# Kernel tuning notes

Hardware: AMD Instinct MI355X
Metric: run time of the kernel (lower is better)

Reference implementation:

```python
import jax, jax.numpy as jnp
import numpy as np

DIM = 64
N_VAR = 60000
N_CON = 40000
N = 100000
E = 500000
NL = 4  # number of MIPGNN layers


def setup_inputs() -> dict:
    key = jax.random.key(0)
    ks = iter(jax.random.split(key, 64))
    def nrm(shape, scale=0.1):
        return jax.random.normal(next(ks), shape, jnp.float32) * scale
    inp = {}
    inp["var_node_features"] = nrm((N_VAR, 1), 1.0)
    inp["con_node_features"] = nrm((N_CON, 1), 1.0)
    inp["edge_features"] = nrm((N, 1), 1.0)
    inp["edge_index"] = jax.random.randint(next(ks), (2, E), 0, N)
    inp["edge_types"] = jax.random.randint(next(ks), (E,), 0, 2)
    inp["assoc_var"] = jnp.arange(N_VAR)
    inp["assoc_con"] = jnp.arange(N_VAR, N)
    # var/con input MLPs
    inp["var_mlp_w1"] = nrm((1, DIM - 2)); inp["var_mlp_b1"] = jnp.zeros((DIM - 2,), jnp.float32)
    inp["var_mlp_w2"] = nrm((DIM - 2, DIM - 2)); inp["var_mlp_b2"] = jnp.zeros((DIM - 2,), jnp.float32)
    inp["con_mlp_w1"] = nrm((1, DIM - 1)); inp["con_mlp_b1"] = jnp.zeros((DIM - 1,), jnp.float32)
    inp["con_mlp_w2"] = nrm((DIM - 1, DIM - 1)); inp["con_mlp_b2"] = jnp.zeros((DIM - 1,), jnp.float32)
    # per-layer MIPGNN params (stacked over NL layers)
    inp["htv_w1"] = nrm((NL, DIM, DIM)); inp["htv_b1"] = jnp.zeros((NL, DIM), jnp.float32)
    inp["htv_w2"] = nrm((NL, DIM, 1)); inp["htv_b2"] = jnp.zeros((NL, 1), jnp.float32)
    inp["w_cons"] = nrm((NL, DIM - 2, DIM - 2))
    inp["w_vars"] = nrm((NL, DIM, DIM))
    inp["bias"] = nrm((NL, DIM))
    # final dense head
    inp["fc1_w"] = nrm((5 * DIM, DIM)); inp["fc1_b"] = jnp.zeros((DIM,), jnp.float32)
    inp["fc2_w"] = nrm((DIM, DIM)); inp["fc2_b"] = jnp.zeros((DIM,), jnp.float32)
    inp["fc3_w"] = nrm((DIM, DIM)); inp["fc3_b"] = jnp.zeros((DIM,), jnp.float32)
    inp["fc4_w"] = nrm((DIM, 1)); inp["fc4_b"] = jnp.zeros((1,), jnp.float32)
    return inp


def _mlp2_relu(x, w1, b1, w2, b2):
    return jax.nn.relu(x @ w1 + b1) @ w2 + b2


def _net_forward(var_node_features, con_node_features, edge_features,
                 var_mlp_w1, var_mlp_b1, var_mlp_w2, var_mlp_b2,
                 con_mlp_w1, con_mlp_b1, con_mlp_w2, con_mlp_b2,
                 htv_w1, htv_b1, htv_w2, htv_b2, w_cons, w_vars, bias,
                 fc1_w, fc1_b, fc2_w, fc2_b, fc3_w, fc3_b, fc4_w, fc4_b,
                 edge_index, edge_types, assoc_var, assoc_con):
    # build initial node features: [var_mlp(v), v, 1] and [con_mlp(c), c]
    ones = jnp.ones_like(var_node_features)
    n = jnp.concatenate([_mlp2_relu(var_node_features, var_mlp_w1, var_mlp_b1, var_mlp_w2, var_mlp_b2),
                         var_node_features, ones], axis=-1)  # [N_VAR, DIM]
    e = jnp.concatenate([_mlp2_relu(con_node_features, con_mlp_w1, con_mlp_b1, con_mlp_w2, con_mlp_b2),
                         con_node_features], axis=-1)         # [N_CON, DIM]
    x = jnp.zeros((N, DIM), jnp.float32).at[assoc_var].set(n).at[assoc_con].set(e)

    src, dst = edge_index[0], edge_index[1]
    et0 = (edge_types == 0)[:, None]          # [E, 1]
    ef_src = edge_features[src]               # [E, 1] (edge_feature indexed by source node)

    xs = [x]
    for l in range(NL):
        xj = xs[-1][src]                      # gather [E, DIM]
        h = jax.nn.sigmoid(xj @ htv_w1[l] + htv_b1[l])
        var_assign = (h @ htv_w2[l] + htv_b2[l]) * ef_src   # [E, 1]
        out0 = jnp.concatenate([xj[:, :-2] @ w_cons[l], xj[:, -2:-1], var_assign], axis=-1)
        out1 = xj @ w_vars[l]
        msg = jnp.where(et0, out0, out1)      # edge-type branching
        aggr = jax.ops.segment_sum(msg, dst, num_segments=N) + bias[l]
        xs.append(jax.nn.relu(aggr))

    xcat = jnp.concatenate(xs, axis=-1)[assoc_var]   # [N_VAR, 5*DIM]
    h = jax.nn.relu(xcat @ fc1_w + fc1_b)
    h = jax.nn.relu(h @ fc2_w + fc2_b)
    h = jax.nn.relu(h @ fc3_w + fc3_b)
    return (h @ fc4_w + fc4_b).squeeze(-1)           # [N_VAR]


def reference(var_node_features, con_node_features, edge_features,
              edge_index, edge_types, assoc_var, assoc_con,
              var_mlp_w1, var_mlp_b1, var_mlp_w2, var_mlp_b2,
              con_mlp_w1, con_mlp_b1, con_mlp_w2, con_mlp_b2,
              htv_w1, htv_b1, htv_w2, htv_b2, w_cons, w_vars, bias,
              fc1_w, fc1_b, fc2_w, fc2_b, fc3_w, fc3_b, fc4_w, fc4_b):
    return _net_forward(var_node_features, con_node_features, edge_features,
                        var_mlp_w1, var_mlp_b1, var_mlp_w2, var_mlp_b2,
                        con_mlp_w1, con_mlp_b1, con_mlp_w2, con_mlp_b2,
                        htv_w1, htv_b1, htv_w2, htv_b2, w_cons, w_vars, bias,
                        fc1_w, fc1_b, fc2_w, fc2_b, fc3_w, fc3_b, fc4_w, fc4_b,
                        edge_index, edge_types, assoc_var, assoc_con)
```

## Files before the change

### kernel.cpp

```cpp
#include <hip/hip_runtime.h>
#include <hip/hip_bf16.h>

typedef unsigned int u32;
typedef unsigned short u16;
typedef __attribute__((ext_vector_type(8))) short frag8;
typedef __attribute__((ext_vector_type(4))) float f32x4;

#define NNODE 100000
#define NVAR  60000
#define NCON  40000
#define NEDGE 500000
#define SLOTCAP 32
#define VAR_BLOCKS 469
#define CON_BLOCKS 313

#define WP_NODE(l)  ((l) * 24576)
#define WP_VARW2    98304
#define WP_CONW2    106496
#define WP_FC1(ph)  (114688 + (ph) * 20480)
#define WP_FC2      155648
#define WP_FC3      163840
#define PREP_TOTAL  86016

__device__ __forceinline__ u16 f2bf(float f) {
  u32 u = __float_as_uint(f);
  u32 r = (u + 0x7fffu + ((u >> 16) & 1u)) >> 16;
  return (u16)r;
}
__device__ __forceinline__ float bf2f(u16 u) { return __uint_as_float(((u32)u) << 16); }
__device__ __forceinline__ float cvlo(u32 p) { return __uint_as_float(p << 16); }
__device__ __forceinline__ float cvhi(u32 p) { return __uint_as_float(p & 0xffff0000u); }
__device__ __forceinline__ float sigmoidf_(float x) {
  return __builtin_amdgcn_rcpf(1.0f + __expf(-x));
}

__global__ __launch_bounds__(256) void k_prep(
    const float* __restrict__ hw1, const float* __restrict__ wco,
    const float* __restrict__ wva, const float* __restrict__ vw2,
    const float* __restrict__ cw2, const float* __restrict__ f1w,
    const float* __restrict__ f2w, const float* __restrict__ f3w,
    u16* __restrict__ wp)
{
  int g = blockIdx.x * 256 + threadIdx.x;
  if (g >= PREP_TOTAL) return;
  float w; u16* base; int k, n, fr_hi, fr_lo;
  if (g < 49152) {
    int l = g / 12288, e = g % 12288;
    base = wp + WP_NODE(l);
    if (e < 4096) {
      k = e >> 6; n = e & 63;
      w = hw1[l * 4096 + e];
      int ksp = k >> 5, nt = n >> 4;
      fr_hi = ksp * 4 + nt;
      fr_lo = (2 + ksp) * 4 + nt;
    } else {
      int e2 = e - 4096;
      int kk = e2 >> 6; n = e2 & 63;
      if (kk < 64) w = (kk < 62 && n < 62) ? wco[l * 3844 + kk * 62 + n] : 0.f;
      else         w = wva[l * 4096 + (kk - 64) * 64 + n];
      k = kk;
      int kkp = kk >> 5, nt = n >> 4;
      fr_hi = 16 + kkp * 4 + nt;
      fr_lo = 16 + (4 + kkp) * 4 + nt;
    }
  } else if (g < 53248) {
    int idx = g - 49152; k = idx >> 6; n = idx & 63;
    w = (k < 62 && n < 62) ? vw2[k * 62 + n] : 0.f;
    base = wp + WP_VARW2;
    int ksp = k >> 5, nt = n >> 4;
    fr_hi = ksp * 4 + nt; fr_lo = (2 + ksp) * 4 + nt;
  } else if (g < 57344) {
    int idx = g - 53248; k = idx >> 6; n = idx & 63;
    w = (k < 63 && n < 63) ? cw2[k * 63 + n] : 0.f;
    base = wp + WP_CONW2;
    int ksp = k >> 5, nt = n >> 4;
    fr_hi = ksp * 4 + nt; fr_lo = (2 + ksp) * 4 + nt;
  } else if (g < 77824) {
    int e = g - 57344; int kk = e >> 6; n = e & 63;
    int ph = (kk >= 160); k = kk - ph * 160;
    w = f1w[(size_t)kk * 64 + n];
    base = wp + WP_FC1(ph);
    int ksp = k >> 5, nt = n >> 4;
    fr_hi = ksp * 4 + nt; fr_lo = (5 + ksp) * 4 + nt;
  } else if (g < 81920) {
    int idx = g - 77824; k = idx >> 6; n = idx & 63;
    w = f2w[idx];
    base = wp + WP_FC2;
    int ksp = k >> 5, nt = n >> 4;
    fr_hi = ksp * 4 + nt; fr_lo = (2 + ksp) * 4 + nt;
  } else {
    int idx = g - 81920; k = idx >> 6; n = idx & 63;
    w = f3w[idx];
    base = wp + WP_FC3;
    int ksp = k >> 5, nt = n >> 4;
    fr_hi = ksp * 4 + nt; fr_lo = (2 + ksp) * 4 + nt;
  }
  u16 hi = f2bf(w);
  u16 lo = f2bf(w - bf2f(hi));
  int lane = (n & 15) | (((k & 31) >> 3) << 4);
  int j = k & 7;
  base[fr_hi * 512 + lane * 8 + j] = hi;
  base[fr_lo * 512 + lane * 8 + j] = lo;
}

__global__ __launch_bounds__(256) void k_init(
    const float* __restrict__ vf, const float* __restrict__ cf,
    const int* __restrict__ avar, const int* __restrict__ acon,
    const float* __restrict__ vw1, const float* __restrict__ vb1, const float* __restrict__ vb2,
    const float* __restrict__ cw1, const float* __restrict__ cb1, const float* __restrict__ cb2,
    const u16* __restrict__ wp, u16* __restrict__ x0, int* __restrict__ cnt)
{
  for (int i = blockIdx.x * 256 + threadIdx.x; i < NNODE; i += gridDim.x * 256) cnt[i] = 0;

  const bool isVar = blockIdx.x < VAR_BLOCKS;
  const int bbase = isVar ? blockIdx.x : (blockIdx.x - VAR_BLOCKS);
  const int nItems = isVar ? NVAR : NCON;
  const int KD = isVar ? 62 : 63;
  const float* in  = isVar ? vf : cf;
  const int*   asc = isVar ? avar : acon;
  const float* w1  = isVar ? vw1 : cw1;
  const float* b1  = isVar ? vb1 : cb1;
  const float* b2  = isVar ? vb2 : cb2;
  const u16*   src = wp + (isVar ? WP_VARW2 : WP_CONW2);

  __shared__ u16 sB[16 * 512];
  __shared__ float sw1[64], sb1[64], sb2[64];
  {
    const uint4* s4 = reinterpret_cast<const uint4*>(src);
    uint4* d4 = reinterpret_cast<uint4*>(sB);
    for (int i = threadIdx.x; i < 1024; i += 256) d4[i] = s4[i];
  }
  if (threadIdx.x < 64) {
    int t = threadIdx.x;
    sw1[t] = (t < KD) ? w1[t] : 0.f;
    sb1[t] = (t < KD) ? b1[t] : 0.f;
    sb2[t] = (t < KD) ? b2[t] : 0.f;
  }
  __syncthreads();

  int wid = threadIdx.x >> 6, lane = threadIdx.x & 63;
  long ib = ((long)bbase * 4 + wid) * 32;
  if (ib >= nItems) return;
  int l15 = lane & 15, lg = lane >> 4;

  float w1r[16], b1r[16];
#pragma unroll
  for (int ks = 0; ks < 2; ++ks)
#pragma unroll
    for (int j = 0; j < 8; ++j) {
      int k = 32 * ks + 8 * lg + j;
      w1r[ks * 8 + j] = sw1[k]; b1r[ks * 8 + j] = sb1[k];
    }

  float v0 = in[ib + l15], v1 = in[ib + 16 + l15];
  frag8 hh[2][2], hl[2][2];
#pragma unroll
  for (int np = 0; np < 2; ++np) {
    float v = np ? v1 : v0;
#pragma unroll
    for (int ks = 0; ks < 2; ++ks) {
      frag8 th, tl;
#pragma unroll
      for (int j = 0; j < 8; ++j) {
        float h = fmaxf(fmaf(v, w1r[ks * 8 + j], b1r[ks * 8 + j]), 0.f);
        u16 hi = f2bf(h);
        u16 lo = f2bf(h - bf2f(hi));
        th[j] = (short)hi; tl[j] = (short)lo;
      }
      hh[np][ks] = th; hl[np][ks] = tl;
    }
  }

  const f32x4 z = {0.f, 0.f, 0.f, 0.f};
  f32x4 acc[4][2];
#pragma unroll
  for (int m = 0; m < 4; ++m)
#pragma unroll
    for (int np = 0; np < 2; ++np) acc[m][np] = z;

#pragma unroll
  for (int ks = 0; ks < 2; ++ks)
#pragma unroll
    for (int m = 0; m < 4; ++m) {
      frag8 bh = *reinterpret_cast<const frag8*>(&sB[((ks * 4 + m) * 512) + lane * 8]);
      frag8 bl = *reinterpret_cast<const frag8*>(&sB[(((2 + ks) * 4 + m) * 512) + lane * 8]);
#pragma unroll
      for (int np = 0; np < 2; ++np) {
        acc[m][np] = __builtin_amdgcn_mfma_f32_16x16x32_bf16(bh, hh[np][ks], acc[m][np], 0, 0, 0);
        acc[m][np] = __builtin_amdgcn_mfma_f32_16x16x32_bf16(bh, hl[np][ks], acc[m][np], 0, 0, 0);
        acc[m][np] = __builtin_amdgcn_mfma_f32_16x16x32_bf16(bl, hh[np][ks], acc[m][np], 0, 0, 0);
      }
    }

#pragma unroll
  for (int np = 0; np < 2; ++np) {
    long r = asc[ib + 16 * np + l15];
    float vv = np ? v1 : v0;
    u16* orow = x0 + r * 64;
#pragma unroll
    for (int m = 0; m < 4; ++m) {
      float o[4];
#pragma unroll
      for (int rr = 0; rr < 4; ++rr) o[rr] = acc[m][np][rr] + sb2[16 * m + 4 * lg + rr];
      if (m == 3 && lg == 3) {
        if (isVar) { o[2] = vv; o[3] = 1.0f; } else { o[3] = vv; }
      }
      u32 p0 = (u32)f2bf(o[0]) | ((u32)f2bf(o[1]) << 16);
      u32 p1 = (u32)f2bf(o[2]) | ((u32)f2bf(o[3]) << 16);
      *reinterpret_cast<uint2*>(orow + 16 * m + 4 * lg) = make_uint2(p0, p1);
    }
  }
}

__global__ __launch_bounds__(256) void k_scatter(
    const int* __restrict__ src, const int* __restrict__ dst,
    const int* __restrict__ et, int* __restrict__ cnt, int* __restrict__ slots)
{
  int e = blockIdx.x * 256 + threadIdx.x;
  if (e >= NEDGE) return;
  int d = dst[e];
  int pos = atomicAdd(&cnt[d], 1);
  if (pos < SLOTCAP) slots[d * SLOTCAP + pos] = src[e] | ((et[e] & 1) << 20);
}

__global__ __launch_bounds__(256) void k_gate(
    const u16* __restrict__ x, const float* __restrict__ ef,
    const u16* __restrict__ wsrc,
    const float* __restrict__ b1, const float* __restrict__ w2,
    const float* __restrict__ b2, float* __restrict__ va)
{
  __shared__ u16 sB[16 * 512];
  __shared__ float sb1[64], sw2[64];
  {
    const uint4* s4 = reinterpret_cast<const uint4*>(wsrc);
    uint4* d4 = reinterpret_cast<uint4*>(sB);
    for (int i = threadIdx.x; i < 1024; i += 256) d4[i] = s4[i];
  }
  if (threadIdx.x < 64) { sb1[threadIdx.x] = b1[threadIdx.x]; sw2[threadIdx.x] = w2[threadIdx.x]; }
  __syncthreads();

  int wid = threadIdx.x >> 6, lane = threadIdx.x & 63;
  long nb = ((long)blockIdx.x * 4 + wid) * 32;
  if (nb >= NNODE) return;
  int l15 = lane & 15, lg = lane >> 4;

  frag8 xf[2][2];
#pragma unroll
  for (int np = 0; np < 2; ++np) {
    const u16* base = x + (nb + 16 * np + l15) * 64 + 8 * lg;
    xf[np][0] = *reinterpret_cast<const frag8*>(base);
    xf[np][1] = *reinterpret_cast<const frag8*>(base + 32);
  }

  const f32x4 z = {0.f, 0.f, 0.f, 0.f};
  f32x4 acc[4][2];
#pragma unroll
  for (int m = 0; m < 4; ++m)
#pragma unroll
    for (int np = 0; np < 2; ++np) acc[m][np] = z;

#pragma unroll
  for (int ks = 0; ks < 2; ++ks)
#pragma unroll
    for (int m = 0; m < 4; ++m) {
      frag8 bh = *reinterpret_cast<const frag8*>(&sB[((ks * 4 + m) * 512) + lane * 8]);
      frag8 bl = *reinterpret_cast<const frag8*>(&sB[(((2 + ks) * 4 + m) * 512) + lane * 8]);
#pragma unroll
      for (int np = 0; np < 2; ++np) {
        acc[m][np] = __builtin_amdgcn_mfma_f32_16x16x32_bf16(bh, xf[np][ks], acc[m][np], 0, 0, 0);
        acc[m][np] = __builtin_amdgcn_mfma_f32_16x16x32_bf16(bl, xf[np][ks], acc[m][np], 0, 0, 0);
      }
    }

  float b2v = b2[0];
#pragma unroll
  for (int np = 0; np < 2; ++np) {
    float p = 0.f;
#pragma unroll
    for (int m = 0; m < 4; ++m)
#pragma unroll
      for (int r = 0; r < 4; ++r)
        p += sigmoidf_(acc[m][np][r] + sb1[16 * m + 4 * lg + r]) * sw2[16 * m + 4 * lg + r];
    p += __shfl_xor(p, 16);
    p += __shfl_xor(p, 32);
    if (lane < 16) {
      long node = nb + 16 * np + lane;
      va[node] = (p + b2v) * ef[node];
    }
  }
}

__global__ __launch_bounds__(256) void k_aggr2(
    const u16* __restrict__ x, const float* __restrict__ va,
    const int* __restrict__ cnt, const int* __restrict__ slots,
    const u16* __restrict__ wsrc,
    const float* __restrict__ bias, u16* __restrict__ xout)
{
  int wid = threadIdx.x >> 6, lane = threadIdx.x & 63;
  int q = lane >> 4, p = lane & 15;
  int nb = (blockIdx.x * 4 + wid) * 16;
  int node = nb + p;
  bool active = (node < NNODE);

  float a0[16], a1[16];
#pragma unroll
  for (int i = 0; i < 16; ++i) { a0[i] = 0.f; a1[i] = 0.f; }
  float sva = 0.f;

  if (active) {
    int deg = cnt[node]; if (deg > SLOTCAP) deg = SLOTCAP;
    const int* sl = slots + (size_t)node * SLOTCAP;
#pragma unroll 1
    for (int j0 = 0; j0 < deg; j0 += 4) {
      int4 sv = *reinterpret_cast<const int4*>(sl + j0);
#pragma unroll
      for (int k = 0; k < 4; ++k) {
        int v = (k == 0) ? sv.x : (k == 1) ? sv.y : (k == 2) ? sv.z : sv.w;
        bool ok = (j0 + k < deg);
        int s = ok ? (v & 0xFFFFF) : 0;
        int t = (v >> 20) & 1;
        const u16* xr = x + (size_t)s * 64 + 8 * q;
        uint4 r0 = *reinterpret_cast<const uint4*>(xr);
        uint4 r1 = *reinterpret_cast<const uint4*>(xr + 32);
        float vg = va[s];
        float m0 = (ok && t == 0) ? 1.f : 0.f;
        float m1 = (ok && t != 0) ? 1.f : 0.f;
        float f[16] = {cvlo(r0.x), cvhi(r0.x), cvlo(r0.y), cvhi(r0.y),
                       cvlo(r0.z), cvhi(r0.z), cvlo(r0.w), cvhi(r0.w),
                       cvlo(r1.x), cvhi(r1.x), cvlo(r1.y), cvhi(r1.y),
                       cvlo(r1.z), cvhi(r1.z), cvlo(r1.w), cvhi(r1.w)};
#pragma unroll
        for (int i = 0; i < 16; ++i) {
          a0[i] = fmaf(f[i], m0, a0[i]);
          a1[i] = fmaf(f[i], m1, a1[i]);
        }
        sva = fmaf(vg, m0, sva);
      }
    }
  }

  float s62 = a0[14];

  frag8 sh[4], sl_[4];
#pragma unroll
  for (int ks = 0; ks < 2; ++ks)
#pragma unroll
    for (int j = 0; j < 8; ++j) {
      float v0 = a0[ks * 8 + j];
      u16 h0 = f2bf(v0);
      sh[ks][j] = (short)h0; sl_[ks][j] = (short)f2bf(v0 - bf2f(h0));
      float v1 = a1[ks * 8 + j];
      u16 h1 = f2bf(v1);
      sh[2 + ks][j] = (short)h1; sl_[2 + ks][j] = (short)f2bf(v1 - bf2f(h1));
    }

  const f32x4 z = {0.f, 0.f, 0.f, 0.f};
  f32x4 acc[4];
#pragma unroll
  for (int m = 0; m < 4; ++m) acc[m] = z;
#pragma unroll
  for (int ks = 0; ks < 4; ++ks)
#pragma unroll
    for (int m = 0; m < 4; ++m) {
      frag8 wh = *reinterpret_cast<const frag8*>(&wsrc[((ks * 4 + m) * 512) + lane * 8]);
      frag8 wl = *reinterpret_cast<const frag8*>(&wsrc[((16 + ks * 4 + m) * 512) + lane * 8]);
      acc[m] = __builtin_amdgcn_mfma_f32_16x16x32_bf16(wh, sh[ks],  acc[m], 0, 0, 0);
      acc[m] = __builtin_amdgcn_mfma_f32_16x16x32_bf16(wh, sl_[ks], acc[m], 0, 0, 0);
      acc[m] = __builtin_amdgcn_mfma_f32_16x16x32_bf16(wl, sh[ks],  acc[m], 0, 0, 0);
    }

  if (!active) return;
  u16* orow = xout + (size_t)node * 64;
#pragma unroll
  for (int m = 0; m < 4; ++m) {
    f32x4 bv = *reinterpret_cast<const f32x4*>(bias + 16 * m + 4 * q);
    float o[4];
#pragma unroll
    for (int r = 0; r < 4; ++r) o[r] = acc[m][r] + bv[r];
    if (m == 3 && q == 3) { o[2] += s62; o[3] += sva; }
    u32 p0 = (u32)f2bf(fmaxf(o[0], 0.f)) | ((u32)f2bf(fmaxf(o[1], 0.f)) << 16);
    u32 p1 = (u32)f2bf(fmaxf(o[2], 0.f)) | ((u32)f2bf(fmaxf(o[3], 0.f)) << 16);
    *reinterpret_cast<uint2*>(orow + 16 * m + 4 * q) = make_uint2(p0, p1);
  }
}

__global__ __launch_bounds__(256) void k_head1(
    const u16* __restrict__ xs, const int* __restrict__ assoc,
    const u16* __restrict__ wp, const float* __restrict__ fb,
    u16* __restrict__ ohi, u16* __restrict__ olo)
{
  __shared__ u16 sB[40 * 512];
  __shared__ float sfb[64];
  if (threadIdx.x < 64) sfb[threadIdx.x] = fb[threadIdx.x];

  int wid = threadIdx.x >> 6, lane = threadIdx.x & 63;
  long ib = ((long)blockIdx.x * 4 + wid) * 32;
  bool act = (ib < NVAR);
  int l15 = lane & 15, lg = lane >> 4;
  long node0 = 0, node1 = 0;
  if (act) { node0 = assoc[ib + l15]; node1 = assoc[ib + 16 + l15]; }

  const f32x4 z = {0.f, 0.f, 0.f, 0.f};
  f32x4 acc[4][2];
#pragma unroll
  for (int m = 0; m < 4; ++m)
#pragma unroll
    for (int np = 0; np < 2; ++np) acc[m][np] = z;

#pragma unroll 1
  for (int ph = 0; ph < 2; ++ph) {
    __syncthreads();
    {
      const uint4* s4 = reinterpret_cast<const uint4*>(wp + WP_FC1(ph));
      uint4* d4 = reinterpret_cast<uint4*>(sB);
      for (int i = threadIdx.x; i < 2560; i += 256) d4[i] = s4[i];
    }
    __syncthreads();
    if (!act) continue;
#pragma unroll
    for (int ks = 0; ks < 5; ++ks) {
      int kg = ph * 160 + ks * 32;
      int pl = kg >> 6, c = (kg & 63) + 8 * lg;
      frag8 a0 = *reinterpret_cast<const frag8*>(xs + ((size_t)pl * NNODE + node0) * 64 + c);
      frag8 a1 = *reinterpret_cast<const frag8*>(xs + ((size_t)pl * NNODE + node1) * 64 + c);
#pragma unroll
      for (int m = 0; m < 4; ++m) {
        frag8 bh = *reinterpret_cast<const frag8*>(&sB[((ks * 4 + m) * 512) + lane * 8]);
        frag8 bl = *reinterpret_cast<const frag8*>(&sB[(((5 + ks) * 4 + m) * 512) + lane * 8]);
        acc[m][0] = __builtin_amdgcn_mfma_f32_16x16x32_bf16(bh, a0, acc[m][0], 0, 0, 0);
        acc[m][0] = __builtin_amdgcn_mfma_f32_16x16x32_bf16(bl, a0, acc[m][0], 0, 0, 0);
        acc[m][1] = __builtin_amdgcn_mfma_f32_16x16x32_bf16(bh, a1, acc[m][1], 0, 0, 0);
        acc[m][1] = __builtin_amdgcn_mfma_f32_16x16x32_bf16(bl, a1, acc[m][1], 0, 0, 0);
      }
    }
  }
  if (!act) return;
#pragma unroll
  for (int np = 0; np < 2; ++np) {
    size_t row = (size_t)(ib + 16 * np + l15) * 64;
#pragma unroll
    for (int m = 0; m < 4; ++m) {
      u16 hi[4], lo[4];
#pragma unroll
      for (int r = 0; r < 4; ++r) {
        float v = fmaxf(acc[m][np][r] + sfb[16 * m + 4 * lg + r], 0.f);
        hi[r] = f2bf(v);
        lo[r] = f2bf(v - bf2f(hi[r]));
      }
      size_t o = row + 16 * m + 4 * lg;
      *reinterpret_cast<uint2*>(ohi + o) =
          make_uint2((u32)hi[0] | ((u32)hi[1] << 16), (u32)hi[2] | ((u32)hi[3] << 16));
      *reinterpret_cast<uint2*>(olo + o) =
          make_uint2((u32)lo[0] | ((u32)lo[1] << 16), (u32)lo[2] | ((u32)lo[3] << 16));
    }
  }
}

__global__ __launch_bounds__(256) void k_dense64(
    const u16* __restrict__ ahi, const u16* __restrict__ alo,
    const u16* __restrict__ wsrc, const float* __restrict__ b,
    u16* __restrict__ ohi, u16* __restrict__ olo)
{
  __shared__ u16 sB[16 * 512];
  __shared__ float sbv[64];
  {
    const uint4* s4 = reinterpret_cast<const uint4*>(wsrc);
    uint4* d4 = reinterpret_cast<uint4*>(sB);
    for (int i = threadIdx.x; i < 1024; i += 256) d4[i] = s4[i];
  }
  if (threadIdx.x < 64) sbv[threadIdx.x] = b[threadIdx.x];
  __syncthreads();

  int wid = threadIdx.x >> 6, lane = threadIdx.x & 63;
  long ib = ((long)blockIdx.x * 4 + wid) * 32;
  if (ib >= NVAR) return;
  int l15 = lane & 15, lg = lane >> 4;

  frag8 xh[2][2], xl[2][2];
#pragma unroll
  for (int np = 0; np < 2; ++np) {
    const u16* bh_ = ahi + (ib + 16 * np + l15) * 64 + 8 * lg;
    const u16* bl_ = alo + (ib + 16 * np + l15) * 64 + 8 * lg;
    xh[np][0] = *reinterpret_cast<const frag8*>(bh_);
    xh[np][1] = *reinterpret_cast<const frag8*>(bh_ + 32);
    xl[np][0] = *reinterpret_cast<const frag8*>(bl_);
    xl[np][1] = *reinterpret_cast<const frag8*>(bl_ + 32);
  }

  const f32x4 z = {0.f, 0.f, 0.f, 0.f};
  f32x4 acc[4][2];
#pragma unroll
  for (int m = 0; m < 4; ++m)
#pragma unroll
    for (int np = 0; np < 2; ++np) acc[m][np] = z;

#pragma unroll
  for (int ks = 0; ks < 2; ++ks)
#pragma unroll
    for (int m = 0; m < 4; ++m) {
      frag8 bh = *reinterpret_cast<const frag8*>(&sB[((ks * 4 + m) * 512) + lane * 8]);
      frag8 bl = *reinterpret_cast<const frag8*>(&sB[(((2 + ks) * 4 + m) * 512) + lane * 8]);
#pragma unroll
      for (int np = 0; np < 2; ++np) {
        acc[m][np] = __builtin_amdgcn_mfma_f32_16x16x32_bf16(bh, xh[np][ks], acc[m][np], 0, 0, 0);
        acc[m][np] = __builtin_amdgcn_mfma_f32_16x16x32_bf16(bh, xl[np][ks], acc[m][np], 0, 0, 0);
        acc[m][np] = __builtin_amdgcn_mfma_f32_16x16x32_bf16(bl, xh[np][ks], acc[m][np], 0, 0, 0);
      }
    }

#pragma unroll
  for (int np = 0; np < 2; ++np) {
    size_t row = (size_t)(ib + 16 * np + l15) * 64;
#pragma unroll
    for (int m = 0; m < 4; ++m) {
      u16 hi[4], lo[4];
#pragma unroll
      for (int r = 0; r < 4; ++r) {
        float v = fmaxf(acc[m][np][r] + sbv[16 * m + 4 * lg + r], 0.f);
        hi[r] = f2bf(v);
        lo[r] = f2bf(v - bf2f(hi[r]));
      }
      size_t o = row + 16 * m + 4 * lg;
      *reinterpret_cast<uint2*>(ohi + o) =
          make_uint2((u32)hi[0] | ((u32)hi[1] << 16), (u32)hi[2] | ((u32)hi[3] << 16));
      *reinterpret_cast<uint2*>(olo + o) =
          make_uint2((u32)lo[0] | ((u32)lo[1] << 16), (u32)lo[2] | ((u32)lo[3] << 16));
    }
  }
}

__global__ __launch_bounds__(256) void k_head4(
    const u16* __restrict__ ahi, const u16* __restrict__ alo,
    const float* __restrict__ w, const float* __restrict__ b,
    float* __restrict__ out)
{
  __shared__ float sw[64];
  if (threadIdx.x < 64) sw[threadIdx.x] = w[threadIdx.x];
  __syncthreads();
  int i = blockIdx.x * 256 + threadIdx.x;
  if (i >= NVAR) return;
  float acc = b[0];
  const uint4* hp = reinterpret_cast<const uint4*>(ahi + (size_t)i * 64);
  const uint4* lp = reinterpret_cast<const uint4*>(alo + (size_t)i * 64);
#pragma unroll
  for (int j = 0; j < 8; ++j) {
    uint4 h = hp[j], l = lp[j];
    acc += (cvlo(h.x) + cvlo(l.x)) * sw[8 * j + 0] + (cvhi(h.x) + cvhi(l.x)) * sw[8 * j + 1];
    acc += (cvlo(h.y) + cvlo(l.y)) * sw[8 * j + 2] + (cvhi(h.y) + cvhi(l.y)) * sw[8 * j + 3];
    acc += (cvlo(h.z) + cvlo(l.z)) * sw[8 * j + 4] + (cvhi(h.z) + cvhi(l.z)) * sw[8 * j + 5];
    acc += (cvlo(h.w) + cvlo(l.w)) * sw[8 * j + 6] + (cvhi(h.w) + cvhi(l.w)) * sw[8 * j + 7];
  }
  out[i] = acc;
}

extern "C" void kernel_launch(void* const* d_in, const int* in_sizes, int n_in,
                              void* d_out, int out_size, void* d_ws, size_t ws_size,
                              hipStream_t stream)
{
  (void)in_sizes; (void)n_in; (void)out_size; (void)ws_size;
  const float* var_nf = (const float*)d_in[0];
  const float* con_nf = (const float*)d_in[1];
  const float* edge_f = (const float*)d_in[2];
  const int*   eidx   = (const int*)d_in[3];
  const int*   etyp   = (const int*)d_in[4];
  const int*   avar   = (const int*)d_in[5];
  const int*   acon   = (const int*)d_in[6];
  const float* vw1 = (const float*)d_in[7];
  const float* vb1 = (const float*)d_in[8];
  const float* vw2 = (const float*)d_in[9];
  const float* vb2 = (const float*)d_in[10];
  const float* cw1 = (const float*)d_in[11];
  const float* cb1 = (const float*)d_in[12];
  const float* cw2 = (const float*)d_in[13];
  const float* cb2 = (const float*)d_in[14];
  const float* hw1 = (const float*)d_in[15];
  const float* hb1 = (const float*)d_in[16];
  const float* hw2 = (const float*)d_in[17];
  const float* hb2 = (const float*)d_in[18];
  const float* wco = (const float*)d_in[19];
  const float* wva = (const float*)d_in[20];
  const float* bia = (const float*)d_in[21];
  const float* f1w = (const float*)d_in[22];
  const float* f1b = (const float*)d_in[23];
  const float* f2w = (const float*)d_in[24];
  const float* f2b = (const float*)d_in[25];
  const float* f3w = (const float*)d_in[26];
  const float* f3b = (const float*)d_in[27];
  const float* f4w = (const float*)d_in[28];
  const float* f4b = (const float*)d_in[29];

  char* ws = (char*)d_ws;
  u16*   xs    = (u16*)ws;
  int*   cnt   = (int*)(ws + 64000000);
  int*   slots = (int*)(ws + 64400000);
  float* va    = (float*)(ws + 77200000);
  u16*   wp    = (u16*)(ws + 77760000);
  u16* hAhi = (u16*)(ws + 78400000);
  u16* hAlo = (u16*)(ws + 86080000);
  u16* hBhi = (u16*)(ws + 93760000);
  u16* hBlo = (u16*)(ws + 101440000);

  const int* esrc = eidx;
  const int* edst = eidx + NEDGE;

  k_prep<<<PREP_TOTAL / 256, 256, 0, stream>>>(hw1, wco, wva, vw2, cw2, f1w, f2w, f3w, wp);
  k_init<<<VAR_BLOCKS + CON_BLOCKS, 256, 0, stream>>>(
      var_nf, con_nf, avar, acon, vw1, vb1, vb2, cw1, cb1, cb2, wp, xs, cnt);
  k_scatter<<<(NEDGE + 255) / 256, 256, 0, stream>>>(esrc, edst, etyp, cnt, slots);

  for (int l = 0; l < 4; ++l) {
    u16* xin  = xs + (size_t)l * NNODE * 64;
    u16* xout = xs + (size_t)(l + 1) * NNODE * 64;
    k_gate<<<(NNODE + 127) / 128, 256, 0, stream>>>(
        xin, edge_f, wp + WP_NODE(l), hb1 + l * 64, hw2 + l * 64, hb2 + l, va);
    k_aggr2<<<(NNODE + 63) / 64, 256, 0, stream>>>(
        xin, va, cnt, slots, wp + WP_NODE(l) + 16 * 512, bia + l * 64, xout);
  }

  k_head1<<<(NVAR + 127) / 128, 256, 0, stream>>>(xs, avar, wp, f1b, hAhi, hAlo);
  k_dense64<<<(NVAR + 127) / 128, 256, 0, stream>>>(hAhi, hAlo, wp + WP_FC2, f2b, hBhi, hBlo);
  k_dense64<<<(NVAR + 127) / 128, 256, 0, stream>>>(hBhi, hBlo, wp + WP_FC3, f3b, hAhi, hAlo);
  k_head4<<<(NVAR + 255) / 256, 256, 0, stream>>>(hAhi, hAlo, f4w, f4b, (float*)d_out);
}
```

Before: 337.4 us.

## Fuse gate MLP into init and aggregation epilogues; fuse fc3 with fc4 head

Removes the standalone k_gate kernel. The next layer's gate value (sigmoid MLP times edge feature) is now computed in the epilogue of k_init and k_aggr2, reading the freshly produced node rows from LDS and ping-ponging between two va buffers. The fc3 dense layer and the final fc4 dot product are merged into one kernel, so the fc3 activations are no longer written out and read back. This saves four kernel launches and a full re-read of the node feature tensor per layer, at the cost of more registers and LDS in k_init and k_aggr2 and gate weights read directly from global memory.

```diff
diff --git a/kernel.cpp b/kernel.cpp
--- a/kernel.cpp
+++ b/kernel.cpp
@@ -13,6 +13,7 @@
 #define SLOTCAP 32
 #define VAR_BLOCKS 469
 #define CON_BLOCKS 313
+#define XPAD 68
 
 #define WP_NODE(l)  ((l) * 24576)
 #define WP_VARW2    98304
@@ -108,7 +109,10 @@
     const int* __restrict__ avar, const int* __restrict__ acon,
     const float* __restrict__ vw1, const float* __restrict__ vb1, const float* __restrict__ vb2,
     const float* __restrict__ cw1, const float* __restrict__ cb1, const float* __restrict__ cb2,
-    const u16* __restrict__ wp, u16* __restrict__ x0, int* __restrict__ cnt)
+    const u16* __restrict__ wp, u16* __restrict__ x0, int* __restrict__ cnt,
+    const float* __restrict__ ef, const float* __restrict__ gb1,
+    const float* __restrict__ gw2, const float* __restrict__ gb2,
+    float* __restrict__ va0)
 {
   for (int i = blockIdx.x * 256 + threadIdx.x; i < NNODE; i += gridDim.x * 256) cnt[i] = 0;
 
@@ -124,6 +128,7 @@
   const u16*   src = wp + (isVar ? WP_VARW2 : WP_CONW2);
 
   __shared__ u16 sB[16 * 512];
+  __shared__ u16 sX[4][32 * XPAD];
   __shared__ float sw1[64], sb1[64], sb2[64];
   {
     const uint4* s4 = reinterpret_cast<const uint4*>(src);
@@ -192,9 +197,11 @@
       }
     }
 
+  long rsave[2];
 #pragma unroll
   for (int np = 0; np < 2; ++np) {
     long r = asc[ib + 16 * np + l15];
+    rsave[np] = r;
     float vv = np ? v1 : v0;
     u16* orow = x0 + r * 64;
 #pragma unroll
@@ -208,7 +215,47 @@
       u32 p0 = (u32)f2bf(o[0]) | ((u32)f2bf(o[1]) << 16);
       u32 p1 = (u32)f2bf(o[2]) | ((u32)f2bf(o[3]) << 16);
       *reinterpret_cast<uint2*>(orow + 16 * m + 4 * lg) = make_uint2(p0, p1);
-    }
+      *reinterpret_cast<uint2*>(&sX[wid][(np * 16 + l15) * XPAD + 16 * m + 4 * lg]) =
+          make_uint2(p0, p1);
+    }
+  }
+  asm volatile("s_waitcnt lgkmcnt(0)" ::: "memory");
+
+  const u16* wg = wp + WP_NODE(0);
+  f32x4 accg[4][2];
+#pragma unroll
+  for (int m = 0; m < 4; ++m)
+#pragma unroll
+    for (int np = 0; np < 2; ++np) accg[m][np] = z;
+#pragma unroll
+  for (int ks = 0; ks < 2; ++ks) {
+    frag8 xg0 = *reinterpret_cast<const frag8*>(&sX[wid][(0 * 16 + l15) * XPAD + ks * 32 + 8 * lg]);
+    frag8 xg1 = *reinterpret_cast<const frag8*>(&sX[wid][(1 * 16 + l15) * XPAD + ks * 32 + 8 * lg]);
+#pragma unroll
+    for (int m = 0; m < 4; ++m) {
+      frag8 wh = *reinterpret_cast<const frag8*>(&wg[((ks * 4 + m) * 512) + lane * 8]);
+      frag8 wl = *reinterpret_cast<const frag8*>(&wg[(((2 + ks) * 4 + m) * 512) + lane * 8]);
+      accg[m][0] = __builtin_amdgcn_mfma_f32_16x16x32_bf16(wh, xg0, accg[m][0], 0, 0, 0);
+      accg[m][0] = __builtin_amdgcn_mfma_f32_16x16x32_bf16(wl, xg0, accg[m][0], 0, 0, 0);
+      accg[m][1] = __builtin_amdgcn_mfma_f32_16x16x32_bf16(wh, xg1, accg[m][1], 0, 0, 0);
+      accg[m][1] = __builtin_amdgcn_mfma_f32_16x16x32_bf16(wl, xg1, accg[m][1], 0, 0, 0);
+    }
+  }
+  float b2v = gb2[0];
+#pragma unroll
+  for (int np = 0; np < 2; ++np) {
+    float p = 0.f;
+#pragma unroll
+    for (int m = 0; m < 4; ++m) {
+      f32x4 b1v = *reinterpret_cast<const f32x4*>(gb1 + 16 * m + 4 * lg);
+      f32x4 w2v = *reinterpret_cast<const f32x4*>(gw2 + 16 * m + 4 * lg);
+#pragma unroll
+      for (int r = 0; r < 4; ++r)
+        p += sigmoidf_(accg[m][np][r] + b1v[r]) * w2v[r];
+    }
+    p += __shfl_xor(p, 16);
+    p += __shfl_xor(p, 32);
+    if (lane < 16) va0[rsave[np]] = (p + b2v) * ef[rsave[np]];
   }
 }
 
@@ -223,79 +270,17 @@
   if (pos < SLOTCAP) slots[d * SLOTCAP + pos] = src[e] | ((et[e] & 1) << 20);
 }
 
-__global__ __launch_bounds__(256) void k_gate(
-    const u16* __restrict__ x, const float* __restrict__ ef,
-    const u16* __restrict__ wsrc,
-    const float* __restrict__ b1, const float* __restrict__ w2,
-    const float* __restrict__ b2, float* __restrict__ va)
-{
-  __shared__ u16 sB[16 * 512];
-  __shared__ float sb1[64], sw2[64];
-  {
-    const uint4* s4 = reinterpret_cast<const uint4*>(wsrc);
-    uint4* d4 = reinterpret_cast<uint4*>(sB);
-    for (int i = threadIdx.x; i < 1024; i += 256) d4[i] = s4[i];
-  }
-  if (threadIdx.x < 64) { sb1[threadIdx.x] = b1[threadIdx.x]; sw2[threadIdx.x] = w2[threadIdx.x]; }
-  __syncthreads();
-
-  int wid = threadIdx.x >> 6, lane = threadIdx.x & 63;
-  long nb = ((long)blockIdx.x * 4 + wid) * 32;
-  if (nb >= NNODE) return;
-  int l15 = lane & 15, lg = lane >> 4;
-
-  frag8 xf[2][2];
-#pragma unroll
-  for (int np = 0; np < 2; ++np) {
-    const u16* base = x + (nb + 16 * np + l15) * 64 + 8 * lg;
-    xf[np][0] = *reinterpret_cast<const frag8*>(base);
-    xf[np][1] = *reinterpret_cast<const frag8*>(base + 32);
-  }
-
-  const f32x4 z = {0.f, 0.f, 0.f, 0.f};
-  f32x4 acc[4][2];
-#pragma unroll
-  for (int m = 0; m < 4; ++m)
-#pragma unroll
-    for (int np = 0; np < 2; ++np) acc[m][np] = z;
-
-#pragma unroll
-  for (int ks = 0; ks < 2; ++ks)
-#pragma unroll
-    for (int m = 0; m < 4; ++m) {
-      frag8 bh = *reinterpret_cast<const frag8*>(&sB[((ks * 4 + m) * 512) + lane * 8]);
-      frag8 bl = *reinterpret_cast<const frag8*>(&sB[(((2 + ks) * 4 + m) * 512) + lane * 8]);
-#pragma unroll
-      for (int np = 0; np < 2; ++np) {
-        acc[m][np] = __builtin_amdgcn_mfma_f32_16x16x32_bf16(bh, xf[np][ks], acc[m][np], 0, 0, 0);
-        acc[m][np] = __builtin_amdgcn_mfma_f32_16x16x32_bf16(bl, xf[np][ks], acc[m][np], 0, 0, 0);
-      }
-    }
-
-  float b2v = b2[0];
-#pragma unroll
-  for (int np = 0; np < 2; ++np) {
-    float p = 0.f;
-#pragma unroll
-    for (int m = 0; m < 4; ++m)
-#pragma unroll
-      for (int r = 0; r < 4; ++r)
-        p += sigmoidf_(acc[m][np][r] + sb1[16 * m + 4 * lg + r]) * sw2[16 * m + 4 * lg + r];
-    p += __shfl_xor(p, 16);
-    p += __shfl_xor(p, 32);
-    if (lane < 16) {
-      long node = nb + 16 * np + lane;
-      va[node] = (p + b2v) * ef[node];
-    }
-  }
-}
-
 __global__ __launch_bounds__(256) void k_aggr2(
     const u16* __restrict__ x, const float* __restrict__ va,
     const int* __restrict__ cnt, const int* __restrict__ slots,
     const u16* __restrict__ wsrc,
-    const float* __restrict__ bias, u16* __restrict__ xout)
+    const float* __restrict__ bias, u16* __restrict__ xout,
+    const u16* __restrict__ w1g,
+    const float* __restrict__ gb1, const float* __restrict__ gw2,
+    const float* __restrict__ gb2, const float* __restrict__ ef,
+    float* __restrict__ va_next)
 {
+  __shared__ u16 sX[4][16 * XPAD];
   int wid = threadIdx.x >> 6, lane = threadIdx.x & 63;
   int q = lane >> 4, p = lane & 15;
   int nb = (blockIdx.x * 4 + wid) * 16;
@@ -369,7 +354,6 @@
       acc[m] = __builtin_amdgcn_mfma_f32_16x16x32_bf16(wl, sh[ks],  acc[m], 0, 0, 0);
     }
 
-  if (!active) return;
   u16* orow = xout + (size_t)node * 64;
 #pragma unroll
   for (int m = 0; m < 4; ++m) {
@@ -380,7 +364,42 @@
     if (m == 3 && q == 3) { o[2] += s62; o[3] += sva; }
     u32 p0 = (u32)f2bf(fmaxf(o[0], 0.f)) | ((u32)f2bf(fmaxf(o[1], 0.f)) << 16);
     u32 p1 = (u32)f2bf(fmaxf(o[2], 0.f)) | ((u32)f2bf(fmaxf(o[3], 0.f)) << 16);
-    *reinterpret_cast<uint2*>(orow + 16 * m + 4 * q) = make_uint2(p0, p1);
+    if (active)
+      *reinterpret_cast<uint2*>(orow + 16 * m + 4 * q) = make_uint2(p0, p1);
+    *reinterpret_cast<uint2*>(&sX[wid][p * XPAD + 16 * m + 4 * q]) = make_uint2(p0, p1);
+  }
+
+  if (w1g == nullptr) return;
+  asm volatile("s_waitcnt lgkmcnt(0)" ::: "memory");
+
+  f32x4 accg[4];
+#pragma unroll
+  for (int m = 0; m < 4; ++m) accg[m] = z;
+#pragma unroll
+  for (int ks = 0; ks < 2; ++ks) {
+    frag8 xg = *reinterpret_cast<const frag8*>(&sX[wid][p * XPAD + ks * 32 + 8 * q]);
+#pragma unroll
+    for (int m = 0; m < 4; ++m) {
+      frag8 wh = *reinterpret_cast<const frag8*>(&w1g[((ks * 4 + m) * 512) + lane * 8]);
+      frag8 wl = *reinterpret_cast<const frag8*>(&w1g[(((2 + ks) * 4 + m) * 512) + lane * 8]);
+      accg[m] = __builtin_amdgcn_mfma_f32_16x16x32_bf16(wh, xg, accg[m], 0, 0, 0);
+      accg[m] = __builtin_amdgcn_mfma_f32_16x16x32_bf16(wl, xg, accg[m], 0, 0, 0);
+    }
+  }
+  float pg = 0.f;
+#pragma unroll
+  for (int m = 0; m < 4; ++m) {
+    f32x4 b1v = *reinterpret_cast<const f32x4*>(gb1 + 16 * m + 4 * q);
+    f32x4 w2v = *reinterpret_cast<const f32x4*>(gw2 + 16 * m + 4 * q);
+#pragma unroll
+    for (int r = 0; r < 4; ++r)
+      pg += sigmoidf_(accg[m][r] + b1v[r]) * w2v[r];
+  }
+  pg += __shfl_xor(pg, 16);
+  pg += __shfl_xor(pg, 32);
+  if (lane < 16 && nb + lane < NNODE) {
+    int n2 = nb + lane;
+    va_next[n2] = (pg + gb2[0]) * ef[n2];
   }
 }
 
@@ -529,28 +548,82 @@
   }
 }
 
-__global__ __launch_bounds__(256) void k_head4(
+__global__ __launch_bounds__(256) void k_dense64o(
     const u16* __restrict__ ahi, const u16* __restrict__ alo,
-    const float* __restrict__ w, const float* __restrict__ b,
+    const u16* __restrict__ wsrc, const float* __restrict__ b,
+    const float* __restrict__ w4, const float* __restrict__ b4,
     float* __restrict__ out)
 {
-  __shared__ float sw[64];
-  if (threadIdx.x < 64) sw[threadIdx.x] = w[threadIdx.x];
+  __shared__ u16 sB[16 * 512];
+  __shared__ float sbv[64], sw4[64];
+  {
+    const uint4* s4 = reinterpret_cast<const uint4*>(wsrc);
+    uint4* d4 = reinterpret_cast<uint4*>(sB);
+    for (int i = threadIdx.x; i < 1024; i += 256) d4[i] = s4[i];
+  }
+  if (threadIdx.x < 64) {
+    sbv[threadIdx.x] = b[threadIdx.x];
+    sw4[threadIdx.x] = w4[threadIdx.x];
+  }
   __syncthreads();
-  int i = blockIdx.x * 256 + threadIdx.x;
-  if (i >= NVAR) return;
-  float acc = b[0];
-  const uint4* hp = reinterpret_cast<const uint4*>(ahi + (size_t)i * 64);
-  const uint4* lp = reinterpret_cast<const uint4*>(alo + (size_t)i * 64);
-#pragma unroll
-  for (int j = 0; j < 8; ++j) {
-    uint4 h = hp[j], l = lp[j];
-    acc += (cvlo(h.x) + cvlo(l.x)) * sw[8 * j + 0] + (cvhi(h.x) + cvhi(l.x)) * sw[8 * j + 1];
-    acc += (cvlo(h.y) + cvlo(l.y)) * sw[8 * j + 2] + (cvhi(h.y) + cvhi(l.y)) * sw[8 * j + 3];
-    acc += (cvlo(h.z) + cvlo(l.z)) * sw[8 * j + 4] + (cvhi(h.z) + cvhi(l.z)) * sw[8 * j + 5];
-    acc += (cvlo(h.w) + cvlo(l.w)) * sw[8 * j + 6] + (cvhi(h.w) + cvhi(l.w)) * sw[8 * j + 7];
-  }
-  out[i] = acc;
+
+  int wid = threadIdx.x >> 6, lane = threadIdx.x & 63;
+  long ib = ((long)blockIdx.x * 4 + wid) * 32;
+  if (ib >= NVAR) return;
+  int l15 = lane & 15, lg = lane >> 4;
+
+  frag8 xh[2][2], xl[2][2];
+#pragma unroll
+  for (int np = 0; np < 2; ++np) {
+    const u16* bh_ = ahi + (ib + 16 * np + l15) * 64 + 8 * lg;
+    const u16* bl_ = alo + (ib + 16 * np + l15) * 64 + 8 * lg;
+    xh[np][0] = *reinterpret_cast<const frag8*>(bh_);
+    xh[np][1] = *reinterpret_cast<const frag8*>(bh_ + 32);
+    xl[np][0] = *reinterpret_cast<const frag8*>(bl_);
+    xl[np][1] = *reinterpret_cast<const frag8*>(bl_ + 32);
+  }
+
+  const f32x4 z = {0.f, 0.f, 0.f, 0.f};
+  f32x4 acc[4][2];
+#pragma unroll
+  for (int m = 0; m < 4; ++m)
+#pragma unroll
+    for (int np = 0; np < 2; ++np) acc[m][np] = z;
+
+#pragma unroll
+  for (int ks = 0; ks < 2; ++ks)
+#pragma unroll
+    for (int m = 0; m < 4; ++m) {
+      frag8 bh = *reinterpret_cast<const frag8*>(&sB[((ks * 4 + m) * 512) + lane * 8]);
+      frag8 bl = *reinterpret_cast<const frag8*>(&sB[(((2 + ks) * 4 + m) * 512) + lane * 8]);
+#pragma unroll
+      for (int np = 0; np < 2; ++np) {
+        acc[m][np] = __builtin_amdgcn_mfma_f32_16x16x32_bf16(bh, xh[np][ks], acc[m][np], 0, 0, 0);
+        acc[m][np] = __builtin_amdgcn_mfma_f32_16x16x32_bf16(bh, xl[np][ks], acc[m][np], 0, 0, 0);
+        acc[m][np] = __builtin_amdgcn_mfma_f32_16x16x32_bf16(bl, xh[np][ks], acc[m][np], 0, 0, 0);
+      }
+    }
+
+  float partial[2] = {0.f, 0.f};
+#pragma unroll
+  for (int np = 0; np < 2; ++np)
+#pragma unroll
+    for (int m = 0; m < 4; ++m)
+#pragma unroll
+      for (int r = 0; r < 4; ++r) {
+        float v = fmaxf(acc[m][np][r] + sbv[16 * m + 4 * lg + r], 0.f);
+        partial[np] = fmaf(v, sw4[16 * m + 4 * lg + r], partial[np]);
+      }
+#pragma unroll
+  for (int np = 0; np < 2; ++np) {
+    partial[np] += __shfl_xor(partial[np], 16);
+    partial[np] += __shfl_xor(partial[np], 32);
+  }
+  if (lane < 16) {
+    float b4v = b4[0];
+    out[ib + lane] = partial[0] + b4v;
+    out[ib + 16 + lane] = partial[1] + b4v;
+  }
 }
 
 extern "C" void kernel_launch(void* const* d_in, const int* in_sizes, int n_in,
@@ -593,8 +666,9 @@
   u16*   xs    = (u16*)ws;
   int*   cnt   = (int*)(ws + 64000000);
   int*   slots = (int*)(ws + 64400000);
-  float* va    = (float*)(ws + 77200000);
-  u16*   wp    = (u16*)(ws + 77760000);
+  float* va0   = (float*)(ws + 77200000);
+  float* va1   = (float*)(ws + 77600000);
+  u16*   wp    = (u16*)(ws + 78000000);
   u16* hAhi = (u16*)(ws + 78400000);
   u16* hAlo = (u16*)(ws + 86080000);
   u16* hBhi = (u16*)(ws + 93760000);
@@ -605,20 +679,27 @@
 
   k_prep<<<PREP_TOTAL / 256, 256, 0, stream>>>(hw1, wco, wva, vw2, cw2, f1w, f2w, f3w, wp);
   k_init<<<VAR_BLOCKS + CON_BLOCKS, 256, 0, stream>>>(
-      var_nf, con_nf, avar, acon, vw1, vb1, vb2, cw1, cb1, cb2, wp, xs, cnt);
+      var_nf, con_nf, avar, acon, vw1, vb1, vb2, cw1, cb1, cb2, wp, xs, cnt,
+      edge_f, hb1, hw2, hb2, va0);
   k_scatter<<<(NEDGE + 255) / 256, 256, 0, stream>>>(esrc, edst, etyp, cnt, slots);
 
   for (int l = 0; l < 4; ++l) {
     u16* xin  = xs + (size_t)l * NNODE * 64;
     u16* xout = xs + (size_t)(l + 1) * NNODE * 64;
-    k_gate<<<(NNODE + 127) / 128, 256, 0, stream>>>(
-        xin, edge_f, wp + WP_NODE(l), hb1 + l * 64, hw2 + l * 64, hb2 + l, va);
+    float* va_in  = (l & 1) ? va1 : va0;
+    float* va_out = (l & 1) ? va0 : va1;
+    bool hasGate = (l < 3);
     k_aggr2<<<(NNODE + 63) / 64, 256, 0, stream>>>(
-        xin, va, cnt, slots, wp + WP_NODE(l) + 16 * 512, bia + l * 64, xout);
+        xin, va_in, cnt, slots, wp + WP_NODE(l) + 16 * 512, bia + l * 64, xout,
+        hasGate ? (wp + WP_NODE(l + 1)) : nullptr,
+        hasGate ? (hb1 + (l + 1) * 64) : nullptr,
+        hasGate ? (hw2 + (l + 1) * 64) : nullptr,
+        hasGate ? (hb2 + (l + 1)) : nullptr,
+        edge_f, va_out);
   }
 
   k_head1<<<(NVAR + 127) / 128, 256, 0, stream>>>(xs, avar, wp, f1b, hAhi, hAlo);
   k_dense64<<<(NVAR + 127) / 128, 256, 0, stream>>>(hAhi, hAlo, wp + WP_FC2, f2b, hBhi, hBlo);
-  k_dense64<<<(NVAR + 127) / 128, 256, 0, stream>>>(hBhi, hBlo, wp + WP_FC3, f3b, hAhi, hAlo);
-  k_head4<<<(NVAR + 255) / 256, 256, 0, stream>>>(hAhi, hAlo, f4w, f4b, (float*)d_out);
-}
+  k_dense64o<<<(NVAR + 127) / 128, 256, 0, stream>>>(hBhi, hBlo, wp + WP_FC3, f3b, f4w, f4b,
+                                                     (float*)d_out);
+}
```

After: 330.6 us. 2.0% less time.
